# Kernel tuning notes

Hardware: AMD Instinct MI355X
Metric: run time of the kernel (lower is better)

The kernel has to match this reference:

```python
import jax, jax.numpy as jnp
import numpy as np

IN_FEATURES = 4096
OUT_FEATURES = 11008
GROUP_SIZE = 128
N_HIGH = 1024   # int(0.25*4096)//8*8
N_LOW = 3072    # (4096-1024)//8*8
M_TOKENS = 64


def unpack_6bit(packed, original_k):
    # packed: [K*3//4, N] uint8 values stored as int32
    _, N = packed.shape
    p = packed.reshape(original_k // 4, 3, N)
    b0, b1, b2 = p[:, 0], p[:, 1], p[:, 2]
    v0 = b0 & 63
    v1 = ((b0 >> 6) & 3) | ((b1 & 15) << 2)
    v2 = ((b1 >> 4) & 15) | ((b2 & 3) << 4)
    v3 = (b2 >> 2) & 63
    return jnp.stack([v0, v1, v2, v3], axis=1).reshape(original_k, N)


def unpack_5bit(packed, original_k):
    # packed: [K*5//8, N]
    _, N = packed.shape
    p = packed.reshape(original_k // 8, 5, N)
    b = [p[:, i] for i in range(5)]
    v0 = b[0] & 31
    v1 = ((b[0] >> 5) & 7) | ((b[1] & 3) << 3)
    v2 = (b[1] >> 2) & 31
    v3 = ((b[1] >> 7) & 1) | ((b[2] & 15) << 1)
    v4 = ((b[2] >> 4) & 15) | ((b[3] & 1) << 4)
    v5 = (b[3] >> 1) & 31
    v6 = ((b[3] >> 6) & 3) | ((b[4] & 7) << 2)
    v7 = (b[4] >> 3) & 31
    return jnp.stack([v0, v1, v2, v3, v4, v5, v6, v7], axis=1).reshape(original_k, N)


def dequant_region(W_q, scales, half_range):
    # W_q: [K, N] ints in [0, 2*half_range]; scales: [num_groups, N]
    K, N = W_q.shape
    G = scales.shape[0]
    Wg = (W_q.astype(jnp.float32) - float(half_range)).reshape(G, GROUP_SIZE, N)
    return (Wg * scales[:, None, :]).reshape(K, N)


def setup_inputs() -> dict:
    key = jax.random.key(0)
    ks = jax.random.split(key, 7)
    x = jax.random.normal(ks[0], (M_TOKENS, IN_FEATURES), dtype=jnp.float32)
    W_high_packed = jax.random.randint(ks[1], (N_HIGH * 3 // 4, OUT_FEATURES), 0, 256, dtype=jnp.int32)
    W_low_packed = jax.random.randint(ks[2], (N_LOW * 5 // 8, OUT_FEATURES), 0, 256, dtype=jnp.int32)
    scales_high = jax.random.uniform(ks[3], (N_HIGH // GROUP_SIZE, OUT_FEATURES), dtype=jnp.float32) * 0.02 + 1e-4
    scales_low = jax.random.uniform(ks[4], (N_LOW // GROUP_SIZE, OUT_FEATURES), dtype=jnp.float32) * 0.02 + 1e-4
    col_indices = jax.random.permutation(ks[5], IN_FEATURES).astype(jnp.int32)
    bias = jax.random.normal(ks[6], (OUT_FEATURES,), dtype=jnp.float32) * 0.02
    return {"x": x, "W_high_packed": W_high_packed, "W_low_packed": W_low_packed,
            "scales_high": scales_high, "scales_low": scales_low,
            "col_indices": col_indices, "bias": bias}


def reference(x, W_high_packed, W_low_packed, scales_high, scales_low, col_indices, bias):
    # Unpack mixed 6-bit / 5-bit weights and group-dequantize.
    Wq_high = unpack_6bit(W_high_packed, N_HIGH)          # [1024, N], 0..63
    Wq_low = unpack_5bit(W_low_packed, N_LOW)             # [3072, N], 0..31
    W_high = dequant_region(Wq_high, scales_high, 31)     # 6-bit half_range = 31
    W_low = dequant_region(Wq_low, scales_low, 15)        # 5-bit half_range = 15
    # Column-sensitivity reorder of activations, then split high/low regions.
    x_perm = x[:, col_indices]                            # [M, K]
    x_high = x_perm[:, :N_HIGH]
    x_low = x_perm[:, N_HIGH:N_HIGH + N_LOW]
    out = x_high @ W_high + x_low @ W_low + bias          # [M, N]
    return out
```

## Files before the change

kernel.cpp:

```cpp
#include <hip/hip_runtime.h>


#define NFEAT 11008
#define KTOT  4096

typedef _Float16 half8 __attribute__((ext_vector_type(8)));
typedef _Float16 half2 __attribute__((ext_vector_type(2)));
typedef float    f32x4 __attribute__((ext_vector_type(4)));

union H8 { half8 v; half2 h[4]; _Float16 e[8]; };

__device__ __forceinline__ half2 dq2(int a, int b, half2 off, half2 s) {
    unsigned u = 0x64006400u | (unsigned)a | ((unsigned)b << 16);
    half2 h = __builtin_bit_cast(half2, u);
    return (h - off) * s;
}

__global__ __launch_bounds__(256) void prep_xfrag(const float* __restrict__ x,
                                                  const int* __restrict__ col,
                                                  _Float16* __restrict__ xfrag) {
    int u  = blockIdx.x * 256 + threadIdx.x;
    int l  = u & 63;
    int mt = (u >> 6) & 3;
    int s  = u >> 8;
    int m  = mt * 16 + (l & 15);
    int kb = s * 32 + ((l >> 4) << 3);
    H8 w;
#pragma unroll
    for (int j = 0; j < 8; ++j)
        w.e[j] = (_Float16)x[m * KTOT + col[kb + j]];
    *(half8*)(xfrag + (size_t)u * 8) = w.v;
}

template <bool HIGH>
__device__ __forceinline__ void run_chunk(const int* __restrict__ W,
                                          const float* __restrict__ S,
                                          const _Float16* __restrict__ xfrag,
                                          int kloc, int sgbase,
                                          int n, int quad, int lane,
                                          f32x4 acc[4]) {
    constexpr int NR = HIGH ? 6 : 5;
    int   raw[2][6];
    float sc[2];
    half8 a[2][4];

    auto issue = [&](int t, int st) {
        const int k0  = kloc + t * 32 + quad * 8;
        const int row = HIGH ? 3 * (k0 >> 2) : 5 * (k0 >> 3);
        const int* p  = W + (size_t)row * NFEAT + n;
#pragma unroll
        for (int r = 0; r < NR; ++r) raw[st][r] = p[(size_t)r * NFEAT];
        sc[st] = S[(size_t)((kloc + t * 32) >> 7) * NFEAT + n];
        const int sg = sgbase + t;
#pragma unroll
        for (int mt = 0; mt < 4; ++mt)
            a[st][mt] = *(const half8*)(xfrag + (size_t)((sg * 4 + mt) * 64 + lane) * 8);
    };

    auto consume = [&](int st) {
        int v0, v1, v2, v3, v4, v5, v6, v7;
        if constexpr (HIGH) {
            int b0 = raw[st][0], b1 = raw[st][1], b2 = raw[st][2],
                b3 = raw[st][3], b4 = raw[st][4], b5 = raw[st][5];
            v0 = b0 & 63;
            v1 = ((b0 >> 6) & 3) | ((b1 & 15) << 2);
            v2 = ((b1 >> 4) & 15) | ((b2 & 3) << 4);
            v3 = (b2 >> 2) & 63;
            v4 = b3 & 63;
            v5 = ((b3 >> 6) & 3) | ((b4 & 15) << 2);
            v6 = ((b4 >> 4) & 15) | ((b5 & 3) << 4);
            v7 = (b5 >> 2) & 63;
        } else {
            int b0 = raw[st][0], b1 = raw[st][1], b2 = raw[st][2],
                b3 = raw[st][3], b4 = raw[st][4];
            v0 = b0 & 31;
            v1 = ((b0 >> 5) & 7) | ((b1 & 3) << 3);
            v2 = (b1 >> 2) & 31;
            v3 = ((b1 >> 7) & 1) | ((b2 & 15) << 1);
            v4 = ((b2 >> 4) & 15) | ((b3 & 1) << 4);
            v5 = (b3 >> 1) & 31;
            v6 = ((b3 >> 6) & 3) | ((b4 & 7) << 2);
            v7 = (b4 >> 3) & 31;
        }
        const _Float16 ofv = HIGH ? (_Float16)1055.0f : (_Float16)1039.0f;
        const half2 off = {ofv, ofv};
        _Float16 s1 = (_Float16)sc[st];
        half2 s2 = {s1, s1};
        H8 w;
        w.h[0] = dq2(v0, v1, off, s2);
        w.h[1] = dq2(v2, v3, off, s2);
        w.h[2] = dq2(v4, v5, off, s2);
        w.h[3] = dq2(v6, v7, off, s2);
#pragma unroll
        for (int mt = 0; mt < 4; ++mt)
            acc[mt] = __builtin_amdgcn_mfma_f32_16x16x32_f16(a[st][mt], w.v, acc[mt], 0, 0, 0);
    };

    issue(0, 0);
#pragma unroll
    for (int t = 0; t < 16; ++t) {
        if (t + 1 < 16) issue(t + 1, (t + 1) & 1);
        consume(t & 1);
    }
}

__global__ __launch_bounds__(256, 4) void gemm_kernel(const int* __restrict__ Wh,
                                                      const int* __restrict__ Wl,
                                                      const float* __restrict__ sh,
                                                      const float* __restrict__ sl,
                                                      const _Float16* __restrict__ xfrag,
                                                      float* __restrict__ dst,
                                                      int nsub, int atomic_mode) {
    const int lane = threadIdx.x & 63;
    const int wave = threadIdx.x >> 6;
    const int quad = lane >> 4;
    const int n    = blockIdx.x * 64 + wave * 16 + (lane & 15);

    f32x4 acc[4];
#pragma unroll
    for (int i = 0; i < 4; ++i) acc[i] = (f32x4){0.f, 0.f, 0.f, 0.f};

    for (int s = 0; s < nsub; ++s) {
        const int kglob  = (blockIdx.y * nsub + s) * 512;
        const int sgbase = kglob >> 5;
        if (kglob < 1024)
            run_chunk<true >(Wh, sh, xfrag, kglob,        sgbase, n, quad, lane, acc);
        else
            run_chunk<false>(Wl, sl, xfrag, kglob - 1024, sgbase, n, quad, lane, acc);
    }

    const int rb = quad << 2;
    if (atomic_mode) {
#pragma unroll
        for (int mt = 0; mt < 4; ++mt)
#pragma unroll
            for (int r = 0; r < 4; ++r)
                atomicAdd(&dst[(size_t)(mt * 16 + rb + r) * NFEAT + n], acc[mt][r]);
    } else {
        float* o = dst + (size_t)blockIdx.y * 64 * NFEAT;
#pragma unroll
        for (int mt = 0; mt < 4; ++mt)
#pragma unroll
            for (int r = 0; r < 4; ++r)
                o[(size_t)(mt * 16 + rb + r) * NFEAT + n] = acc[mt][r];
    }
}

__global__ __launch_bounds__(256) void reduce_out(const float* __restrict__ part,
                                                  const float* __restrict__ bias,
                                                  float* __restrict__ out, int P) {
    const int idx = blockIdx.x * 256 + threadIdx.x;
    const int f   = idx * 4;
    const int nn  = f % NFEAT;
    f32x4 s = *(const f32x4*)(bias + nn);
    for (int p = 0; p < P; ++p)
        s += *(const f32x4*)(part + (size_t)p * 704512 + f);
    *(f32x4*)(out + f) = s;
}

__global__ __launch_bounds__(256) void init_bias(const float* __restrict__ bias,
                                                 float* __restrict__ out) {
    const int idx = blockIdx.x * 256 + threadIdx.x;
    out[idx] = bias[idx % NFEAT];
}

extern "C" void kernel_launch(void* const* d_in, const int* in_sizes, int n_in,
                              void* d_out, int out_size, void* d_ws, size_t ws_size,
                              hipStream_t stream) {
    const float* x    = (const float*)d_in[0];
    const int*   Wh   = (const int*)d_in[1];
    const int*   Wl   = (const int*)d_in[2];
    const float* sh   = (const float*)d_in[3];
    const float* sl   = (const float*)d_in[4];
    const int*   col  = (const int*)d_in[5];
    const float* bias = (const float*)d_in[6];
    float* out = (float*)d_out;

    _Float16* xfrag = (_Float16*)d_ws;
    const size_t xb      = (size_t)64 * KTOT * sizeof(_Float16);
    const size_t pstride = (size_t)64 * NFEAT;

    prep_xfrag<<<128, 256, 0, stream>>>(x, col, xfrag);

    if (ws_size >= xb + 8 * pstride * sizeof(float)) {
        float* part = (float*)((char*)d_ws + xb);
        gemm_kernel<<<dim3(172, 8), 256, 0, stream>>>(Wh, Wl, sh, sl, xfrag, part, 1, 0);
        reduce_out<<<688, 256, 0, stream>>>(part, bias, out, 8);
    } else if (ws_size >= xb + 4 * pstride * sizeof(float)) {
        float* part = (float*)((char*)d_ws + xb);
        gemm_kernel<<<dim3(172, 4), 256, 0, stream>>>(Wh, Wl, sh, sl, xfrag, part, 2, 0);
        reduce_out<<<688, 256, 0, stream>>>(part, bias, out, 4);
    } else {
        init_bias<<<2752, 256, 0, stream>>>(bias, out);
        gemm_kernel<<<dim3(172, 8), 256, 0, stream>>>(Wh, Wl, sh, sl, xfrag, out, 1, 1);
    }
}
```

Baseline: 195.7 us.

## Deepen software pipeline to two-batch double buffering with wider loads in flight

Restructures the per-chunk loop so each stage loads two 32-wide k-slices (weights, scale, activation fragments). Two such stages are kept in flight and consumed alternately under a non-unrolled loop, in place of the single-step lookahead. This is meant to hide more global-memory latency per wave. It raises register use, so launch bounds drop from 4 to 3 blocks per SM, trading occupancy for memory-level parallelism. The scale is loaded once per pair of slices, relying on pairs not straddling a 128-group.

```diff
diff --git a/kernel.cpp b/kernel.cpp
--- a/kernel.cpp
+++ b/kernel.cpp
@@ -33,35 +33,47 @@
 }
 
 template <bool HIGH>
-__device__ __forceinline__ void run_chunk(const int* __restrict__ W,
-                                          const float* __restrict__ S,
-                                          const _Float16* __restrict__ xfrag,
-                                          int kloc, int sgbase,
-                                          int n, int quad, int lane,
-                                          f32x4 acc[4]) {
+struct Stage {
+    int   raw[HIGH ? 12 : 10];
+    half8 a[8];
+    float sc;
+};
+
+template <bool HIGH>
+__device__ __forceinline__ void issue_batch(const int* __restrict__ Wlane,
+                                            const float* __restrict__ Slane,
+                                            const _Float16* __restrict__ Abase,
+                                            int b, Stage<HIGH>& S) {
+    constexpr int NR   = HIGH ? 6 : 5;
+    constexpr int RPSG = HIGH ? 24 : 20;
+#pragma unroll
+    for (int s = 0; s < 2; ++s) {
+        const int* p = Wlane + (size_t)(b * 2 * RPSG + s * RPSG) * NFEAT;
+#pragma unroll
+        for (int r = 0; r < NR; ++r)
+            S.raw[s * NR + r] = p[(size_t)r * NFEAT];
+    }
+    S.sc = Slane[(size_t)(b >> 1) * NFEAT];
+#pragma unroll
+    for (int s = 0; s < 2; ++s)
+#pragma unroll
+        for (int mt = 0; mt < 4; ++mt)
+            S.a[s * 4 + mt] = *(const half8*)(Abase + ((size_t)(b * 2 + s) * 4 + mt) * 512);
+}
+
+template <bool HIGH>
+__device__ __forceinline__ void consume_batch(const Stage<HIGH>& S, f32x4 acc[4]) {
     constexpr int NR = HIGH ? 6 : 5;
-    int   raw[2][6];
-    float sc[2];
-    half8 a[2][4];
-
-    auto issue = [&](int t, int st) {
-        const int k0  = kloc + t * 32 + quad * 8;
-        const int row = HIGH ? 3 * (k0 >> 2) : 5 * (k0 >> 3);
-        const int* p  = W + (size_t)row * NFEAT + n;
-#pragma unroll
-        for (int r = 0; r < NR; ++r) raw[st][r] = p[(size_t)r * NFEAT];
-        sc[st] = S[(size_t)((kloc + t * 32) >> 7) * NFEAT + n];
-        const int sg = sgbase + t;
-#pragma unroll
-        for (int mt = 0; mt < 4; ++mt)
-            a[st][mt] = *(const half8*)(xfrag + (size_t)((sg * 4 + mt) * 64 + lane) * 8);
-    };
-
-    auto consume = [&](int st) {
+    const _Float16 ofv = HIGH ? (_Float16)1055.0f : (_Float16)1039.0f;
+    const half2 off = {ofv, ofv};
+    const _Float16 s1 = (_Float16)S.sc;
+    const half2 s2 = {s1, s1};
+#pragma unroll
+    for (int s = 0; s < 2; ++s) {
         int v0, v1, v2, v3, v4, v5, v6, v7;
         if constexpr (HIGH) {
-            int b0 = raw[st][0], b1 = raw[st][1], b2 = raw[st][2],
-                b3 = raw[st][3], b4 = raw[st][4], b5 = raw[st][5];
+            int b0 = S.raw[s * 6 + 0], b1 = S.raw[s * 6 + 1], b2 = S.raw[s * 6 + 2],
+                b3 = S.raw[s * 6 + 3], b4 = S.raw[s * 6 + 4], b5 = S.raw[s * 6 + 5];
             v0 = b0 & 63;
             v1 = ((b0 >> 6) & 3) | ((b1 & 15) << 2);
             v2 = ((b1 >> 4) & 15) | ((b2 & 3) << 4);
@@ -71,8 +83,8 @@
             v6 = ((b4 >> 4) & 15) | ((b5 & 3) << 4);
             v7 = (b5 >> 2) & 63;
         } else {
-            int b0 = raw[st][0], b1 = raw[st][1], b2 = raw[st][2],
-                b3 = raw[st][3], b4 = raw[st][4];
+            int b0 = S.raw[s * 5 + 0], b1 = S.raw[s * 5 + 1], b2 = S.raw[s * 5 + 2],
+                b3 = S.raw[s * 5 + 3], b4 = S.raw[s * 5 + 4];
             v0 = b0 & 31;
             v1 = ((b0 >> 5) & 7) | ((b1 & 3) << 3);
             v2 = (b1 >> 2) & 31;
@@ -82,10 +94,6 @@
             v6 = ((b3 >> 6) & 3) | ((b4 & 7) << 2);
             v7 = (b4 >> 3) & 31;
         }
-        const _Float16 ofv = HIGH ? (_Float16)1055.0f : (_Float16)1039.0f;
-        const half2 off = {ofv, ofv};
-        _Float16 s1 = (_Float16)sc[st];
-        half2 s2 = {s1, s1};
         H8 w;
         w.h[0] = dq2(v0, v1, off, s2);
         w.h[1] = dq2(v2, v3, off, s2);
@@ -93,18 +101,37 @@
         w.h[3] = dq2(v6, v7, off, s2);
 #pragma unroll
         for (int mt = 0; mt < 4; ++mt)
-            acc[mt] = __builtin_amdgcn_mfma_f32_16x16x32_f16(a[st][mt], w.v, acc[mt], 0, 0, 0);
-    };
-
-    issue(0, 0);
-#pragma unroll
-    for (int t = 0; t < 16; ++t) {
-        if (t + 1 < 16) issue(t + 1, (t + 1) & 1);
-        consume(t & 1);
-    }
-}
-
-__global__ __launch_bounds__(256, 4) void gemm_kernel(const int* __restrict__ Wh,
+            acc[mt] = __builtin_amdgcn_mfma_f32_16x16x32_f16(S.a[s * 4 + mt], w.v, acc[mt], 0, 0, 0);
+    }
+}
+
+template <bool HIGH>
+__device__ __forceinline__ void run_chunk(const int* __restrict__ W,
+                                          const float* __restrict__ Sg,
+                                          const _Float16* __restrict__ xfrag,
+                                          int kloc, int sgbase,
+                                          int n, int quad, int lane,
+                                          f32x4 acc[4]) {
+    const int row0 = HIGH ? (3 * (kloc >> 2) + 6 * quad) : (5 * (kloc >> 3) + 5 * quad);
+    const int* Wlane       = W + (size_t)row0 * NFEAT + n;
+    const float* Slane     = Sg + (size_t)(kloc >> 7) * NFEAT + n;
+    const _Float16* Abase  = xfrag + (size_t)sgbase * 4 * 512 + lane * 8;
+
+    Stage<HIGH> S0, S1;
+    issue_batch<HIGH>(Wlane, Slane, Abase, 0, S0);
+    issue_batch<HIGH>(Wlane, Slane, Abase, 1, S1);
+#pragma unroll 1
+    for (int b = 0; b < 6; b += 2) {
+        consume_batch<HIGH>(S0, acc);
+        issue_batch<HIGH>(Wlane, Slane, Abase, b + 2, S0);
+        consume_batch<HIGH>(S1, acc);
+        issue_batch<HIGH>(Wlane, Slane, Abase, b + 3, S1);
+    }
+    consume_batch<HIGH>(S0, acc);
+    consume_batch<HIGH>(S1, acc);
+}
+
+__global__ __launch_bounds__(256, 3) void gemm_kernel(const int* __restrict__ Wh,
                                                       const int* __restrict__ Wl,
                                                       const float* __restrict__ sh,
                                                       const float* __restrict__ sl,
```

New measurement: 191.4 us. 1.02x faster.

## Stage packed weight tiles into LDS via direct global-to-LDS loads with swizzle

Applied to the files above, without the earlier changes.

Replaces the per-lane strided global loads of packed weight bytes with cooperative 16-byte global_load_lds transfers into a rotated/swizzled shared-memory tile, then each lane reads its bytes from LDS. The work is reorganised into 8 steps of 64 K each with block-wide barriers, and the register double-buffering of weights and activations is removed. The aim is to make the weight fetch fully coalesced and wide. In exchange it adds barriers, drops the software prefetch overlap, and removes the 4-way split fallback path.

```diff
diff --git a/kernel.cpp b/kernel.cpp
--- a/kernel.cpp
+++ b/kernel.cpp
@@ -15,6 +15,11 @@
     half2 h = __builtin_bit_cast(half2, u);
     return (h - off) * s;
 }
+
+#define GLOAD_LDS16(gp, lp)                                             \
+    __builtin_amdgcn_global_load_lds(                                   \
+        (const __attribute__((address_space(1))) void*)(gp),            \
+        (__attribute__((address_space(3))) void*)(lp), 16, 0, 0)
 
 __global__ __launch_bounds__(256) void prep_xfrag(const float* __restrict__ x,
                                                   const int* __restrict__ col,
@@ -32,101 +37,104 @@
     *(half8*)(xfrag + (size_t)u * 8) = w.v;
 }
 
-template <bool HIGH>
-__device__ __forceinline__ void run_chunk(const int* __restrict__ W,
-                                          const float* __restrict__ S,
-                                          const _Float16* __restrict__ xfrag,
-                                          int kloc, int sgbase,
-                                          int n, int quad, int lane,
-                                          f32x4 acc[4]) {
-    constexpr int NR = HIGH ? 6 : 5;
-    int   raw[2][6];
-    float sc[2];
-    half8 a[2][4];
-
-    auto issue = [&](int t, int st) {
-        const int k0  = kloc + t * 32 + quad * 8;
-        const int row = HIGH ? 3 * (k0 >> 2) : 5 * (k0 >> 3);
-        const int* p  = W + (size_t)row * NFEAT + n;
-#pragma unroll
-        for (int r = 0; r < NR; ++r) raw[st][r] = p[(size_t)r * NFEAT];
-        sc[st] = S[(size_t)((kloc + t * 32) >> 7) * NFEAT + n];
-        const int sg = sgbase + t;
-#pragma unroll
-        for (int mt = 0; mt < 4; ++mt)
-            a[st][mt] = *(const half8*)(xfrag + (size_t)((sg * 4 + mt) * 64 + lane) * 8);
-    };
-
-    auto consume = [&](int st) {
-        int v0, v1, v2, v3, v4, v5, v6, v7;
-        if constexpr (HIGH) {
-            int b0 = raw[st][0], b1 = raw[st][1], b2 = raw[st][2],
-                b3 = raw[st][3], b4 = raw[st][4], b5 = raw[st][5];
-            v0 = b0 & 63;
-            v1 = ((b0 >> 6) & 3) | ((b1 & 15) << 2);
-            v2 = ((b1 >> 4) & 15) | ((b2 & 3) << 4);
-            v3 = (b2 >> 2) & 63;
-            v4 = b3 & 63;
-            v5 = ((b3 >> 6) & 3) | ((b4 & 15) << 2);
-            v6 = ((b4 >> 4) & 15) | ((b5 & 3) << 4);
-            v7 = (b5 >> 2) & 63;
-        } else {
-            int b0 = raw[st][0], b1 = raw[st][1], b2 = raw[st][2],
-                b3 = raw[st][3], b4 = raw[st][4];
-            v0 = b0 & 31;
-            v1 = ((b0 >> 5) & 7) | ((b1 & 3) << 3);
-            v2 = (b1 >> 2) & 31;
-            v3 = ((b1 >> 7) & 1) | ((b2 & 15) << 1);
-            v4 = ((b2 >> 4) & 15) | ((b3 & 1) << 4);
-            v5 = (b3 >> 1) & 31;
-            v6 = ((b3 >> 6) & 3) | ((b4 & 7) << 2);
-            v7 = (b4 >> 3) & 31;
-        }
-        const _Float16 ofv = HIGH ? (_Float16)1055.0f : (_Float16)1039.0f;
-        const half2 off = {ofv, ofv};
-        _Float16 s1 = (_Float16)sc[st];
-        half2 s2 = {s1, s1};
-        H8 w;
-        w.h[0] = dq2(v0, v1, off, s2);
-        w.h[1] = dq2(v2, v3, off, s2);
-        w.h[2] = dq2(v4, v5, off, s2);
-        w.h[3] = dq2(v6, v7, off, s2);
-#pragma unroll
-        for (int mt = 0; mt < 4; ++mt)
-            acc[mt] = __builtin_amdgcn_mfma_f32_16x16x32_f16(a[st][mt], w.v, acc[mt], 0, 0, 0);
-    };
-
-    issue(0, 0);
-#pragma unroll
-    for (int t = 0; t < 16; ++t) {
-        if (t + 1 < 16) issue(t + 1, (t + 1) & 1);
-        consume(t & 1);
-    }
-}
-
 __global__ __launch_bounds__(256, 4) void gemm_kernel(const int* __restrict__ Wh,
                                                       const int* __restrict__ Wl,
                                                       const float* __restrict__ sh,
                                                       const float* __restrict__ sl,
                                                       const _Float16* __restrict__ xfrag,
                                                       float* __restrict__ dst,
-                                                      int nsub, int atomic_mode) {
+                                                      int atomic_mode) {
+    const int n0   = blockIdx.x * 64;
+    const int ky   = blockIdx.y;
     const int lane = threadIdx.x & 63;
     const int wave = threadIdx.x >> 6;
     const int quad = lane >> 4;
-    const int n    = blockIdx.x * 64 + wave * 16 + (lane & 15);
+    const int nl   = lane & 15;
+    const int n    = n0 + wave * 16 + nl;
+
+    const bool high  = (ky < 2);
+    const int  kloc0 = high ? ky * 512 : (ky * 512 - 1024);
+
+    const int*   Wb = high ? Wh : Wl;
+    const float* Sb = high ? sh : sl;
+    const int NI  = high ? 12 : 10;
+    const int RPT = high ? 48 : 40;
+    const int R00 = high ? 3 * (kloc0 >> 2) : 5 * (kloc0 >> 3);
+
+    __shared__ int lds[48 * 64];
 
     f32x4 acc[4];
 #pragma unroll
     for (int i = 0; i < 4; ++i) acc[i] = (f32x4){0.f, 0.f, 0.f, 0.f};
 
-    for (int s = 0; s < nsub; ++s) {
-        const int kglob  = (blockIdx.y * nsub + s) * 512;
-        const int sgbase = kglob >> 5;
-        if (kglob < 1024)
-            run_chunk<true >(Wh, sh, xfrag, kglob,        sgbase, n, quad, lane, acc);
-        else
-            run_chunk<false>(Wl, sl, xfrag, kglob - 1024, sgbase, n, quad, lane, acc);
+    const int srow = lane >> 4;
+    const int spos = lane & 15;
+    const int cneed = wave * 4 + (nl >> 2);
+
+    const _Float16 ofv = high ? (_Float16)1055.0f : (_Float16)1039.0f;
+    const half2 off = {ofv, ofv};
+
+#pragma unroll 1
+    for (int t = 0; t < 8; ++t) {
+        const int Rt = R00 + t * RPT;
+        for (int i = wave; i < NI; i += 4) {
+            const int r  = 4 * i + srow;
+            const int cg = (spos - r) & 15;
+            const int* gp = Wb + (size_t)(Rt + r) * NFEAT + n0 + cg * 4;
+            GLOAD_LDS16(gp, &lds[i * 256]);
+        }
+        const float scf = Sb[(size_t)((kloc0 + t * 64) >> 7) * NFEAT + n];
+        __syncthreads();
+
+        const _Float16 s1 = (_Float16)scf;
+        const half2 s2 = {s1, s1};
+        const int sgb = ky * 16 + t * 2;
+#pragma unroll
+        for (int s = 0; s < 2; ++s) {
+            const int r0 = high ? (24 * s + 6 * quad) : (20 * s + 5 * quad);
+            const int NR = high ? 6 : 5;
+            int b[6];
+#pragma unroll
+            for (int j = 0; j < 6; ++j) {
+                if (j < NR) {
+                    const int r = r0 + j;
+                    const int p = (cneed + r) & 15;
+                    b[j] = lds[r * 64 + p * 4 + (nl & 3)];
+                }
+            }
+            int v0, v1, v2, v3, v4, v5, v6, v7;
+            if (high) {
+                v0 = b[0] & 63;
+                v1 = ((b[0] >> 6) & 3) | ((b[1] & 15) << 2);
+                v2 = ((b[1] >> 4) & 15) | ((b[2] & 3) << 4);
+                v3 = (b[2] >> 2) & 63;
+                v4 = b[3] & 63;
+                v5 = ((b[3] >> 6) & 3) | ((b[4] & 15) << 2);
+                v6 = ((b[4] >> 4) & 15) | ((b[5] & 3) << 4);
+                v7 = (b[5] >> 2) & 63;
+            } else {
+                v0 = b[0] & 31;
+                v1 = ((b[0] >> 5) & 7) | ((b[1] & 3) << 3);
+                v2 = (b[1] >> 2) & 31;
+                v3 = ((b[1] >> 7) & 1) | ((b[2] & 15) << 1);
+                v4 = ((b[2] >> 4) & 15) | ((b[3] & 1) << 4);
+                v5 = (b[3] >> 1) & 31;
+                v6 = ((b[3] >> 6) & 3) | ((b[4] & 7) << 2);
+                v7 = (b[4] >> 3) & 31;
+            }
+            H8 w;
+            w.h[0] = dq2(v0, v1, off, s2);
+            w.h[1] = dq2(v2, v3, off, s2);
+            w.h[2] = dq2(v4, v5, off, s2);
+            w.h[3] = dq2(v6, v7, off, s2);
+            const int sg = sgb + s;
+#pragma unroll
+            for (int mt = 0; mt < 4; ++mt) {
+                half8 a = *(const half8*)(xfrag + ((size_t)(sg * 4 + mt) * 64 + lane) * 8);
+                acc[mt] = __builtin_amdgcn_mfma_f32_16x16x32_f16(a, w.v, acc[mt], 0, 0, 0);
+            }
+        }
+        __syncthreads();
     }
 
     const int rb = quad << 2;
@@ -137,7 +145,7 @@
             for (int r = 0; r < 4; ++r)
                 atomicAdd(&dst[(size_t)(mt * 16 + rb + r) * NFEAT + n], acc[mt][r]);
     } else {
-        float* o = dst + (size_t)blockIdx.y * 64 * NFEAT;
+        float* o = dst + (size_t)ky * 64 * NFEAT;
 #pragma unroll
         for (int mt = 0; mt < 4; ++mt)
 #pragma unroll
@@ -184,14 +192,10 @@
 
     if (ws_size >= xb + 8 * pstride * sizeof(float)) {
         float* part = (float*)((char*)d_ws + xb);
-        gemm_kernel<<<dim3(172, 8), 256, 0, stream>>>(Wh, Wl, sh, sl, xfrag, part, 1, 0);
+        gemm_kernel<<<dim3(172, 8), 256, 0, stream>>>(Wh, Wl, sh, sl, xfrag, part, 0);
         reduce_out<<<688, 256, 0, stream>>>(part, bias, out, 8);
-    } else if (ws_size >= xb + 4 * pstride * sizeof(float)) {
-        float* part = (float*)((char*)d_ws + xb);
-        gemm_kernel<<<dim3(172, 4), 256, 0, stream>>>(Wh, Wl, sh, sl, xfrag, part, 2, 0);
-        reduce_out<<<688, 256, 0, stream>>>(part, bias, out, 4);
     } else {
         init_bias<<<2752, 256, 0, stream>>>(bias, out);
-        gemm_kernel<<<dim3(172, 8), 256, 0, stream>>>(Wh, Wl, sh, sl, xfrag, out, 1, 1);
+        gemm_kernel<<<dim3(172, 8), 256, 0, stream>>>(Wh, Wl, sh, sl, xfrag, out, 1);
     }
 }
```

After: 184.7 us. 5.6% less time.
